# Kernel optimization log

Hardware: AMD Instinct MI355X
Metric: run time of the kernel (lower is better)

Reference implementation:

```python
import jax, jax.numpy as jnp
import numpy as np

B, S, D, H = 2, 2048, 2048, 16
HD = D // H
ROPE_BASE = 10000.0
N_DOCS = 8


def setup_inputs() -> dict:
    key = jax.random.key(0)
    ks = jax.random.split(key, 7)
    scale = 1.0 / np.sqrt(D)
    x = jax.random.normal(ks[0], (B, S, D), dtype=jnp.float32)
    doc_ids = jnp.sort(jax.random.randint(ks[1], (B, S), 0, N_DOCS), axis=1)
    Wq = jax.random.normal(ks[2], (D, D), dtype=jnp.float32) * scale
    Wk = jax.random.normal(ks[3], (D, D), dtype=jnp.float32) * scale
    Wv = jax.random.normal(ks[4], (D, D), dtype=jnp.float32) * scale
    Wo = jax.random.normal(ks[5], (D, D), dtype=jnp.float32) * scale
    bo = jax.random.normal(ks[6], (D,), dtype=jnp.float32) * 0.01
    return {"x": x, "doc_ids": doc_ids, "Wq": Wq, "Wk": Wk, "Wv": Wv, "Wo": Wo, "bo": bo}


def _rotate_half(t):
    # interleaved pairs: (x0,x1,x2,x3,...) -> (-x1,x0,-x3,x2,...)
    t1 = t[..., 0::2]
    t2 = t[..., 1::2]
    return jnp.stack((-t2, t1), axis=-1).reshape(t.shape)


def _doc_position_ids(doc_ids):
    b, s = doc_ids.shape
    boundary = jnp.concatenate(
        [jnp.ones((b, 1), dtype=bool), doc_ids[:, 1:] != doc_ids[:, :-1]], axis=1)
    ar = jnp.arange(s)[None, :]
    boundary_pos = jnp.where(boundary, ar, 0)
    last_boundary = jax.lax.cummax(boundary_pos, axis=1)
    return ar - last_boundary  # position within each document


def reference(x, doc_ids, Wq, Wk, Wv, Wo, bo):
    b, s, d = x.shape
    h, hd = H, HD

    q = (x @ Wq).reshape(b, s, h, hd).transpose(0, 2, 1, 3)  # [b,h,s,hd]
    k = (x @ Wk).reshape(b, s, h, hd).transpose(0, 2, 1, 3)
    v = (x @ Wv).reshape(b, s, h, hd).transpose(0, 2, 1, 3)

    # doc-aware RoPE: positions reset at document boundaries
    pos = _doc_position_ids(doc_ids).astype(jnp.float32)  # [b,s]
    inv_freq = 1.0 / (ROPE_BASE ** (jnp.arange(0, hd, 2, dtype=jnp.float32) / hd))
    freqs = pos[..., None] * inv_freq  # [b,s,hd/2]
    cos = jnp.repeat(jnp.cos(freqs), 2, axis=-1)[:, None]  # [b,1,s,hd]
    sin = jnp.repeat(jnp.sin(freqs), 2, axis=-1)[:, None]
    q = q * cos + _rotate_half(q) * sin
    k = k * cos + _rotate_half(k) * sin

    scores = jnp.einsum("bhqd,bhkd->bhqk", q, k)
    # doc-blockwise causal mask: attend only to j<=i within same document
    same_doc = doc_ids[:, :, None] == doc_ids[:, None, :]  # [b,s,s] (i,j)
    allowed = jnp.tril(same_doc)[:, None]  # [b,1,s,s]
    inv_scale = 1.0 / np.sqrt(hd)
    scores = jnp.where(allowed, scores * inv_scale, -jnp.inf)
    attn = jax.nn.softmax(scores, axis=-1)

    ctx = jnp.einsum("bhqk,bhkd->bhqd", attn, v)
    ctx = ctx.transpose(0, 2, 1, 3).reshape(b, s, d)
    return ctx @ Wo + bo
```

## Files before the change

kernel.cpp:

```cpp
#include <hip/hip_runtime.h>
#include <hip/hip_bf16.h>

#define Dd 2048
#define Ss 2048
#define Bb 2
#define Hh 16
#define HDd 128
#define BSs (Bb*Ss)
#define NTILES 32

typedef __bf16 bf16;
typedef __bf16 bf16x8 __attribute__((ext_vector_type(8)));
typedef __bf16 bf16x4 __attribute__((ext_vector_type(4)));
typedef float f32x4 __attribute__((ext_vector_type(4)));

__device__ __forceinline__ void gload_lds16(const void* g, void* l) {
  __builtin_amdgcn_global_load_lds((__attribute__((address_space(1))) void*)(g),
                                   (__attribute__((address_space(3))) void*)(l), 16, 0, 0);
}

template <int N>
__device__ __forceinline__ void waitv() {
  if constexpr (N == 0) asm volatile("s_waitcnt vmcnt(0)" ::: "memory");
  else if constexpr (N == 2) asm volatile("s_waitcnt vmcnt(2)" ::: "memory");
  else if constexpr (N == 4) asm volatile("s_waitcnt vmcnt(4)" ::: "memory");
  else if constexpr (N == 6) asm volatile("s_waitcnt vmcnt(6)" ::: "memory");
  else if constexpr (N == 8) asm volatile("s_waitcnt vmcnt(8)" ::: "memory");
  else if constexpr (N == 10) asm volatile("s_waitcnt vmcnt(10)" ::: "memory");
}

__global__ void k_cvtx(const float* __restrict__ x, bf16* __restrict__ xb) {
  int i = (blockIdx.x * 256 + threadIdx.x) * 4;
  f32x4 v = *(const f32x4*)(x + i);
  bf16x4 o;
  o[0] = (bf16)v[0]; o[1] = (bf16)v[1]; o[2] = (bf16)v[2]; o[3] = (bf16)v[3];
  *(bf16x4*)(xb + i) = o;
}

__global__ void k_tw(const float* __restrict__ W0, const float* __restrict__ W1,
                     const float* __restrict__ W2, const float* __restrict__ W3,
                     bf16* __restrict__ T0, bf16* __restrict__ T1,
                     bf16* __restrict__ T2, bf16* __restrict__ T3) {
  const float* W; bf16* T;
  switch (blockIdx.z) {
    case 0: W = W0; T = T0; break;
    case 1: W = W1; T = T1; break;
    case 2: W = W2; T = T2; break;
    default: W = W3; T = T3; break;
  }
  __shared__ float t[64][65];
  int n0 = blockIdx.x * 64, k0 = blockIdx.y * 64;
  int tid = threadIdx.x;
#pragma unroll
  for (int rr = 0; rr < 4; rr++) {
    int r = (tid >> 4) + rr * 16;
    f32x4 vv = *(const f32x4*)(W + (size_t)(k0 + r) * Dd + n0 + (tid & 15) * 4);
#pragma unroll
    for (int j = 0; j < 4; j++) t[r][(tid & 15) * 4 + j] = vv[j];
  }
  __syncthreads();
#pragma unroll
  for (int rr = 0; rr < 4; rr++) {
    int n = rr * 16 + (tid >> 4);
    int kb = (tid & 15) * 4;
    bf16x4 o;
#pragma unroll
    for (int j = 0; j < 4; j++) o[j] = (bf16)t[kb + j][n];
    *(bf16x4*)(T + (size_t)(n0 + n) * Dd + k0 + kb) = o;
  }
}

__global__ void k_pos(const int* __restrict__ doc, int* __restrict__ pos) {
  int b = blockIdx.x;
  __shared__ int bp[2][Ss];
  const int* db = doc + (size_t)b * Ss;
  for (int i = threadIdx.x; i < Ss; i += 1024) {
    int bd = (i == 0) || (db[i] != db[i - 1]);
    bp[0][i] = bd ? i : 0;
  }
  __syncthreads();
  int src = 0;
  for (int off = 1; off < Ss; off <<= 1) {
    for (int i = threadIdx.x; i < Ss; i += 1024) {
      int v = bp[src][i];
      if (i >= off) v = max(v, bp[src][i - off]);
      bp[1 - src][i] = v;
    }
    __syncthreads();
    src = 1 - src;
  }
  for (int i = threadIdx.x; i < Ss; i += 1024)
    pos[(size_t)b * Ss + i] = i - bp[src][i];
}

__device__ __forceinline__ bf16x8 lds_frag(const char* buf, int row, int cb) {
  return *(const bf16x8*)(buf + row * 128 + (cb ^ ((row & 7) << 4)));
}

__device__ __forceinline__ void stage_slot128(const bf16* gA, const bf16* gB,
                                              int m0, int n0, int t, int slot, int buf,
                                              char* AL, char* BL, int tid) {
  const char* gp; char* l; int rbase;
  char* bufA = AL + (size_t)buf * 16384;
  char* bufB = BL + (size_t)buf * 32768;
  if (slot == 0)      { gp = (const char*)gA; l = bufA;         rbase = m0; }
  else if (slot == 1) { gp = (const char*)gB; l = bufB;         rbase = n0; }
  else                { gp = (const char*)gB; l = bufB + 16384; rbase = n0 + 128; }
  int ktb = t * 128;
#pragma unroll
  for (int p = 0; p < 2; p++) {
    int o = p * 8192 + tid * 16;
    int r = o >> 7, cb = o & 127;
    gload_lds16(gp + (size_t)(rbase + r) * 4096 + ktb + (cb ^ ((r & 7) << 4)), l + o);
  }
}

template <bool STAGE, int WV0, int WV1>
__device__ __forceinline__ void do_tile128(const bf16* gA, const bf16* gB, int m0, int n0,
                                           int t, int bi, int b2, char* AL, char* BL, int tid,
                                           int wr, int wc, int ln, int g,
                                           f32x4 acc[4][4]) {
  const char* tileA = AL + (size_t)bi * 16384;
  const char* tileB = BL + (size_t)bi * 32768;
  bf16x8 af[4][2], bf_[2][2];

#pragma unroll
  for (int mq = 0; mq < 4; mq++)
#pragma unroll
    for (int kk = 0; kk < 2; kk++)
      af[mq][kk] = lds_frag(tileA, wr * 64 + mq * 16 + ln, kk * 64 + g * 16);
#pragma unroll
  for (int nq = 0; nq < 2; nq++)
#pragma unroll
    for (int kk = 0; kk < 2; kk++)
      bf_[nq][kk] = lds_frag(tileB, wc * 32 + nq * 16 + ln, kk * 64 + g * 16);
  if (STAGE) {
    stage_slot128(gA, gB, m0, n0, t + 2, 0, b2, AL, BL, tid);
    stage_slot128(gA, gB, m0, n0, t + 2, 1, b2, AL, BL, tid);
  }
  waitv<WV0>();
  __builtin_amdgcn_s_barrier();
  __builtin_amdgcn_s_setprio(1);
#pragma unroll
  for (int mq = 0; mq < 4; mq++)
#pragma unroll
    for (int nq = 0; nq < 2; nq++)
#pragma unroll
      for (int kk = 0; kk < 2; kk++)
        acc[mq][nq] = __builtin_amdgcn_mfma_f32_16x16x32_bf16(af[mq][kk], bf_[nq][kk], acc[mq][nq], 0, 0, 0);
  __builtin_amdgcn_s_setprio(0);
  __builtin_amdgcn_s_barrier();

#pragma unroll
  for (int nq = 0; nq < 2; nq++)
#pragma unroll
    for (int kk = 0; kk < 2; kk++)
      bf_[nq][kk] = lds_frag(tileB, 128 + wc * 32 + nq * 16 + ln, kk * 64 + g * 16);
  if (STAGE)
    stage_slot128(gA, gB, m0, n0, t + 2, 2, b2, AL, BL, tid);
  waitv<WV1>();
  __builtin_amdgcn_s_barrier();
  __builtin_amdgcn_s_setprio(1);
#pragma unroll
  for (int mq = 0; mq < 4; mq++)
#pragma unroll
    for (int nq = 0; nq < 2; nq++)
#pragma unroll
      for (int kk = 0; kk < 2; kk++)
        acc[mq][2 + nq] = __builtin_amdgcn_mfma_f32_16x16x32_bf16(af[mq][kk], bf_[nq][kk], acc[mq][2 + nq], 0, 0, 0);
  __builtin_amdgcn_s_setprio(0);
  __builtin_amdgcn_s_barrier();
}

__device__ __forceinline__ void gemm128_core(const bf16* gA, const bf16* gB,
                                             int m0, int n0, char* AL, char* BL,
                                             f32x4 acc[4][4]) {
  const int tid = threadIdx.x;
  const int l = tid & 63, w = tid >> 6;
  const int wr = w >> 2, wc = w & 3;
  const int g = l >> 4, ln = l & 15;
  f32x4 z = {0.f, 0.f, 0.f, 0.f};
#pragma unroll
  for (int i = 0; i < 4; i++)
#pragma unroll
    for (int n = 0; n < 4; n++) acc[i][n] = z;

  stage_slot128(gA, gB, m0, n0, 0, 0, 0, AL, BL, tid);
  stage_slot128(gA, gB, m0, n0, 0, 1, 0, AL, BL, tid);
  stage_slot128(gA, gB, m0, n0, 0, 2, 0, AL, BL, tid);
  stage_slot128(gA, gB, m0, n0, 1, 0, 1, AL, BL, tid);
  stage_slot128(gA, gB, m0, n0, 1, 1, 1, AL, BL, tid);
  stage_slot128(gA, gB, m0, n0, 1, 2, 1, AL, BL, tid);
  waitv<8>();
  __builtin_amdgcn_s_barrier();

  int bi = 0, b2 = 2;
  for (int t = 0; t < NTILES - 2; t++) {
    do_tile128<true, 10, 8>(gA, gB, m0, n0, t, bi, b2, AL, BL, tid, wr, wc, ln, g, acc);
    bi = (bi == 2) ? 0 : bi + 1;
    b2 = (b2 == 2) ? 0 : b2 + 1;
  }
  do_tile128<false, 6, 2>(gA, gB, m0, n0, NTILES - 2, bi, 0, AL, BL, tid, wr, wc, ln, g, acc);
  bi = (bi == 2) ? 0 : bi + 1;
  do_tile128<false, 0, -1>(gA, gB, m0, n0, NTILES - 1, bi, 0, AL, BL, tid, wr, wc, ln, g, acc);
}

__global__ __launch_bounds__(512, 2) void k_qkv128(const bf16* __restrict__ xb,
                                                   const bf16* __restrict__ wqkvt,
                                                   const int* __restrict__ pos,
                                                   bf16* __restrict__ q,
                                                   bf16* __restrict__ k,
                                                   bf16* __restrict__ vt) {
  __shared__ char SLM[147456];
  char* AL = SLM;
  char* BL = SLM + 49152;
  int bid = blockIdx.x;
  int idx = (bid & 7) * 96 + (bid >> 3);
  int mt = idx / 24, nt = idx % 24;
  int m0 = mt * 128, n0 = nt * 256;

  f32x4 acc[4][4];
  gemm128_core(xb, wqkvt, m0, n0, AL, BL, acc);

  const int tid = threadIdx.x;
  const int l = tid & 63, w = tid >> 6;
  const int wr = w >> 2, wc = w & 3, g = l >> 4, ln = l & 15;
  int z = n0 >> 11;
  int n0l = n0 & 2047;
  int bix = m0 >> 11;
  int sl0 = m0 & 2047;

  if (z == 2) {
#pragma unroll
    for (int mq = 0; mq < 4; mq++) {
      int sl = sl0 + wr * 64 + mq * 16 + g * 4;
#pragma unroll
      for (int ni = 0; ni < 4; ni++) {
        int col = n0l + (ni >> 1) * 128 + wc * 32 + (ni & 1) * 16 + ln;
        int h = col >> 7, hd = col & 127;
        bf16x4 o;
#pragma unroll
        for (int r2 = 0; r2 < 4; r2++) o[r2] = (bf16)acc[mq][ni][r2];
        *(bf16x4*)(vt + (((size_t)(bix * Hh + h) * HDd + hd) * Ss + sl)) = o;
      }
    }
  } else {
    bf16* dst = (z == 0) ? q : k;
    float* T = (float*)SLM;
    const float c1 = 0.14391156642398168f;
    int cg = (tid & 31) * 8;
    int hb = n0l + cg;
    int hh = hb >> 7, hd0 = hb & 127;
    float fr[4];
#pragma unroll
    for (int pr = 0; pr < 4; pr++)
      fr[pr] = __expf(-(float)((hd0 >> 1) + pr) * c1);

#pragma unroll
    for (int pass = 0; pass < 2; pass++) {
      __syncthreads();
      if (wr == pass) {
#pragma unroll
        for (int mq = 0; mq < 4; mq++) {
#pragma unroll
          for (int ni = 0; ni < 4; ni++) {
            int c = (ni >> 1) * 128 + wc * 32 + (ni & 1) * 16 + ln;
            int rb = mq * 16 + g * 4;
#pragma unroll
            for (int r2 = 0; r2 < 4; r2++)
              T[(rb + r2) * 260 + c] = acc[mq][ni][r2];
          }
        }
      }
      __syncthreads();
#pragma unroll
      for (int j = 0; j < 4; j++) {
        int r = j * 16 + (tid >> 5);
        int sg = m0 + pass * 64 + r;
        float p = (float)pos[sg];
        f32x4 v0 = *(const f32x4*)(T + r * 260 + cg);
        f32x4 v1 = *(const f32x4*)(T + r * 260 + cg + 4);
        float e0[4] = {v0[0], v0[2], v1[0], v1[2]};
        float e1[4] = {v0[1], v0[3], v1[1], v1[3]};
        int s = sg & 2047;
        bf16x8 o;
#pragma unroll
        for (int pr = 0; pr < 4; pr++) {
          float ang = p * fr[pr];
          float sn, cs;
          __sincosf(ang, &sn, &cs);
          o[2 * pr]     = (bf16)(e0[pr] * cs - e1[pr] * sn);
          o[2 * pr + 1] = (bf16)(e1[pr] * cs + e0[pr] * sn);
        }
        *(bf16x8*)(dst + (((size_t)(bix * Hh + hh) * Ss + s) * HDd + hd0)) = o;
      }
    }
  }
}

__global__ __launch_bounds__(512, 2) void k_out128(const bf16* __restrict__ ctx,
                                                   const bf16* __restrict__ wot,
                                                   const float* __restrict__ bo,
                                                   float* __restrict__ outp) {
  __shared__ char AL[49152];
  __shared__ char BL[98304];
  int bid = blockIdx.x;
  int x = bid & 7, j = bid >> 3;
  int mt = (x >> 1) * 8 + (j >> 2);
  int nt = (x & 1) * 4 + (j & 3);
  int m0 = mt * 128, n0 = nt * 256;

  f32x4 acc[4][4];
  gemm128_core(ctx, wot, m0, n0, AL, BL, acc);

  const int l = threadIdx.x & 63, w = threadIdx.x >> 6;
  const int wr = w >> 2, wc = w & 3, g = l >> 4, ln = l & 15;
  float bov[4];
#pragma unroll
  for (int ni = 0; ni < 4; ni++)
    bov[ni] = bo[n0 + (ni >> 1) * 128 + wc * 32 + (ni & 1) * 16 + ln];
#pragma unroll
  for (int mq = 0; mq < 4; mq++)
#pragma unroll
    for (int r2 = 0; r2 < 4; r2++) {
      int row = m0 + wr * 64 + mq * 16 + g * 4 + r2;
#pragma unroll
      for (int ni = 0; ni < 4; ni++) {
        int col = n0 + (ni >> 1) * 128 + wc * 32 + (ni & 1) * 16 + ln;
        outp[(size_t)row * Dd + col] = acc[mq][ni][r2] + bov[ni];
      }
    }
}

__global__ __launch_bounds__(256) void k_attn(const bf16* __restrict__ q,
                                              const bf16* __restrict__ k,
                                              const bf16* __restrict__ vt,
                                              const int* __restrict__ pos,
                                              bf16* __restrict__ ctx) {
  __shared__ bf16 Ks[64 * 128];
  __shared__ bf16 Vts[128 * 64];
  __shared__ bf16 Pw[4][16 * 64];
  int bh = blockIdx.y;
  int b = bh >> 4, h = bh & 15;
  int qt = blockIdx.x, q0 = qt * 64;
  const int tid = threadIdx.x, l = tid & 63, w = tid >> 6, g = l >> 4, ln = l & 15;
  const bf16* qb = q + (size_t)bh * Ss * HDd;
  const bf16* kb = k + (size_t)bh * Ss * HDd;
  const bf16* vb = vt + (size_t)bh * Ss * HDd;

  bf16x8 qf[4];
  int qr = q0 + w * 16 + ln;
#pragma unroll
  for (int ks = 0; ks < 4; ks++)
    qf[ks] = *(const bf16x8*)(qb + (size_t)qr * HDd + ks * 32 + 8 * g);

  int rrow[4], dstart[4];
  float m[4], lsum[4];
#pragma unroll
  for (int r2 = 0; r2 < 4; r2++) {
    rrow[r2] = q0 + w * 16 + 4 * g + r2;
    dstart[r2] = rrow[r2] - pos[(size_t)b * Ss + rrow[r2]];
    m[r2] = -1e30f;
    lsum[r2] = 0.f;
  }
  f32x4 oacc[8];
  f32x4 z = {0.f, 0.f, 0.f, 0.f};
#pragma unroll
  for (int n = 0; n < 8; n++) oacc[n] = z;

  int kt_start = (q0 - pos[(size_t)b * Ss + q0]) >> 6;
  const float iscale = 0.08838834764831845f;

  for (int kt = kt_start; kt <= qt; kt++) {
    int kv0 = kt * 64;
#pragma unroll
    for (int i2 = 0; i2 < 4; i2++) {
      int o = i2 * 4096 + w * 1024 + l * 16;
      int rk = o >> 8, cbk = o & 255;
      gload_lds16((const char*)kb + (size_t)(kv0 + rk) * 256 + cbk,
                  (char*)Ks + i2 * 4096 + w * 1024);
      int rv = o >> 7, cbv = o & 127;
      gload_lds16((const char*)vb + (size_t)rv * (Ss * 2) + (size_t)kv0 * 2 + cbv,
                  (char*)Vts + i2 * 4096 + w * 1024);
    }
    __syncthreads();

    f32x4 sc[4];
#pragma unroll
    for (int n = 0; n < 4; n++) {
      f32x4 a = z;
#pragma unroll
      for (int ks = 0; ks < 4; ks++) {
        bf16x8 bfrag = *(const bf16x8*)(Ks + (n * 16 + ln) * 128 + ks * 32 + 8 * g);
        a = __builtin_amdgcn_mfma_f32_16x16x32_bf16(qf[ks], bfrag, a, 0, 0, 0);
      }
      sc[n] = a;
    }

    float pmax[4] = {-1e30f, -1e30f, -1e30f, -1e30f};
    float pv[4][4];
#pragma unroll
    for (int n = 0; n < 4; n++) {
      int kvc = kv0 + n * 16 + ln;
#pragma unroll
      for (int r2 = 0; r2 < 4; r2++) {
        bool ok = (kvc <= rrow[r2]) && (kvc >= dstart[r2]);
        float sv = ok ? sc[n][r2] * iscale : -1e30f;
        pv[n][r2] = sv;
        pmax[r2] = fmaxf(pmax[r2], sv);
      }
    }
#pragma unroll
    for (int off = 1; off < 16; off <<= 1)
#pragma unroll
      for (int r2 = 0; r2 < 4; r2++)
        pmax[r2] = fmaxf(pmax[r2], __shfl_xor(pmax[r2], off, 64));

    float alpha[4];
#pragma unroll
    for (int r2 = 0; r2 < 4; r2++) {
      float mn = fmaxf(m[r2], pmax[r2]);
      alpha[r2] = __expf(m[r2] - mn);
      m[r2] = mn;
    }

    float rs[4] = {0.f, 0.f, 0.f, 0.f};
#pragma unroll
    for (int n = 0; n < 4; n++) {
      int kvc = kv0 + n * 16 + ln;
#pragma unroll
      for (int r2 = 0; r2 < 4; r2++) {
        bool ok = (kvc <= rrow[r2]) && (kvc >= dstart[r2]);
        float p = ok ? __expf(pv[n][r2] - m[r2]) : 0.f;
        rs[r2] += p;
        Pw[w][(4 * g + r2) * 64 + n * 16 + ln] = (bf16)p;
      }
    }
#pragma unroll
    for (int off = 1; off < 16; off <<= 1)
#pragma unroll
      for (int r2 = 0; r2 < 4; r2++) rs[r2] += __shfl_xor(rs[r2], off, 64);
#pragma unroll
    for (int r2 = 0; r2 < 4; r2++) lsum[r2] = lsum[r2] * alpha[r2] + rs[r2];
#pragma unroll
    for (int n = 0; n < 8; n++)
#pragma unroll
      for (int r2 = 0; r2 < 4; r2++) oacc[n][r2] *= alpha[r2];
    __syncthreads();

#pragma unroll
    for (int n = 0; n < 8; n++) {
#pragma unroll
      for (int ks = 0; ks < 2; ks++) {
        bf16x8 pa = *(const bf16x8*)(&Pw[w][ln * 64 + ks * 32 + 8 * g]);
        bf16x8 vfr = *(const bf16x8*)(Vts + (n * 16 + ln) * 64 + ks * 32 + 8 * g);
        oacc[n] = __builtin_amdgcn_mfma_f32_16x16x32_bf16(pa, vfr, oacc[n], 0, 0, 0);
      }
    }
    __syncthreads();
  }

#pragma unroll
  for (int n = 0; n < 8; n++)
#pragma unroll
    for (int r2 = 0; r2 < 4; r2++) {
      float val = oacc[n][r2] / lsum[r2];
      ctx[((size_t)(b * Ss + rrow[r2])) * Dd + h * HDd + n * 16 + ln] = (bf16)val;
    }
}

extern "C" void kernel_launch(void* const* d_in, const int* in_sizes, int n_in,
                              void* d_out, int out_size, void* d_ws, size_t ws_size,
                              hipStream_t stream) {
  const float* x = (const float*)d_in[0];
  const int* doc = (const int*)d_in[1];
  const float* Wq = (const float*)d_in[2];
  const float* Wk = (const float*)d_in[3];
  const float* Wv = (const float*)d_in[4];
  const float* Wo = (const float*)d_in[5];
  const float* bo = (const float*)d_in[6];
  float* outp = (float*)d_out;

  char* ws = (char*)d_ws;
  size_t off = 0;
  auto alloc = [&](size_t bytes) {
    char* p = ws + off;
    off += (bytes + 255) & ~(size_t)255;
    return p;
  };
  bf16* xb = (bf16*)alloc((size_t)BSs * Dd * 2);
  bf16* wqkvt = (bf16*)alloc((size_t)3 * Dd * Dd * 2);
  bf16* wot = (bf16*)alloc((size_t)Dd * Dd * 2);
  bf16* qd = (bf16*)alloc((size_t)BSs * Dd * 2);
  bf16* kd = (bf16*)alloc((size_t)BSs * Dd * 2);
  bf16* vtd = (bf16*)alloc((size_t)BSs * Dd * 2);
  bf16* ctxd = (bf16*)alloc((size_t)BSs * Dd * 2);
  int* pos = (int*)alloc((size_t)BSs * 4);

  k_cvtx<<<(BSs * Dd) / 1024, 256, 0, stream>>>(x, xb);
  k_tw<<<dim3(Dd / 64, Dd / 64, 4), 256, 0, stream>>>(
      Wq, Wk, Wv, Wo, wqkvt, wqkvt + (size_t)Dd * Dd, wqkvt + (size_t)2 * Dd * Dd, wot);
  k_pos<<<Bb, 1024, 0, stream>>>(doc, pos);
  k_qkv128<<<dim3(768), 512, 0, stream>>>(xb, wqkvt, pos, qd, kd, vtd);
  k_attn<<<dim3(Ss / 64, Bb * Hh), 256, 0, stream>>>(qd, kd, vtd, pos, ctxd);
  k_out128<<<dim3(256), 512, 0, stream>>>(ctxd, wot, bo, outp);
}
```

Before: 227.0 us.

## Restructure GEMM main loop into single-phase tiles with one barrier per k-step

Replaces the two-phase per-k-tile GEMM schedule (separate B halves, two barriers and two waits) with one stage of the full A and B tiles per k-step. Each warp now reads four A and four B fragments per k-half and issues a 4x4 MFMA block, with a single vmcnt wait and barrier per tile. The loop is unrolled by three to fix triple-buffer indices, and the output-GEMM block-to-tile mapping changes. This aims to cut barrier and wait overhead, at the cost of higher register pressure and less overlap of loads with compute inside a tile.

```diff
diff --git a/kernel.cpp b/kernel.cpp
--- a/kernel.cpp
+++ b/kernel.cpp
@@ -7,7 +7,7 @@
 #define Hh 16
 #define HDd 128
 #define BSs (Bb*Ss)
-#define NTILES 32
+#define NTIL 32
 
 typedef __bf16 bf16;
 typedef __bf16 bf16x8 __attribute__((ext_vector_type(8)));
@@ -22,11 +22,7 @@
 template <int N>
 __device__ __forceinline__ void waitv() {
   if constexpr (N == 0) asm volatile("s_waitcnt vmcnt(0)" ::: "memory");
-  else if constexpr (N == 2) asm volatile("s_waitcnt vmcnt(2)" ::: "memory");
-  else if constexpr (N == 4) asm volatile("s_waitcnt vmcnt(4)" ::: "memory");
   else if constexpr (N == 6) asm volatile("s_waitcnt vmcnt(6)" ::: "memory");
-  else if constexpr (N == 8) asm volatile("s_waitcnt vmcnt(8)" ::: "memory");
-  else if constexpr (N == 10) asm volatile("s_waitcnt vmcnt(10)" ::: "memory");
 }
 
 __global__ void k_cvtx(const float* __restrict__ x, bf16* __restrict__ xb) {
@@ -93,88 +89,64 @@
     pos[(size_t)b * Ss + i] = i - bp[src][i];
 }
 
-__device__ __forceinline__ bf16x8 lds_frag(const char* buf, int row, int cb) {
-  return *(const bf16x8*)(buf + row * 128 + (cb ^ ((row & 7) << 4)));
-}
-
-__device__ __forceinline__ void stage_slot128(const bf16* gA, const bf16* gB,
-                                              int m0, int n0, int t, int slot, int buf,
-                                              char* AL, char* BL, int tid) {
-  const char* gp; char* l; int rbase;
-  char* bufA = AL + (size_t)buf * 16384;
-  char* bufB = BL + (size_t)buf * 32768;
-  if (slot == 0)      { gp = (const char*)gA; l = bufA;         rbase = m0; }
-  else if (slot == 1) { gp = (const char*)gB; l = bufB;         rbase = n0; }
-  else                { gp = (const char*)gB; l = bufB + 16384; rbase = n0 + 128; }
+__device__ __forceinline__ void stage64(const char* gA, const char* gB,
+                                        int m0, int n0, int t, int buf,
+                                        char* AL, char* BL, int tid) {
   int ktb = t * 128;
 #pragma unroll
   for (int p = 0; p < 2; p++) {
     int o = p * 8192 + tid * 16;
     int r = o >> 7, cb = o & 127;
-    gload_lds16(gp + (size_t)(rbase + r) * 4096 + ktb + (cb ^ ((r & 7) << 4)), l + o);
-  }
-}
-
-template <bool STAGE, int WV0, int WV1>
-__device__ __forceinline__ void do_tile128(const bf16* gA, const bf16* gB, int m0, int n0,
-                                           int t, int bi, int b2, char* AL, char* BL, int tid,
-                                           int wr, int wc, int ln, int g,
-                                           f32x4 acc[4][4]) {
-  const char* tileA = AL + (size_t)bi * 16384;
-  const char* tileB = BL + (size_t)bi * 32768;
-  bf16x8 af[4][2], bf_[2][2];
-
-#pragma unroll
-  for (int mq = 0; mq < 4; mq++)
-#pragma unroll
-    for (int kk = 0; kk < 2; kk++)
-      af[mq][kk] = lds_frag(tileA, wr * 64 + mq * 16 + ln, kk * 64 + g * 16);
-#pragma unroll
-  for (int nq = 0; nq < 2; nq++)
-#pragma unroll
-    for (int kk = 0; kk < 2; kk++)
-      bf_[nq][kk] = lds_frag(tileB, wc * 32 + nq * 16 + ln, kk * 64 + g * 16);
-  if (STAGE) {
-    stage_slot128(gA, gB, m0, n0, t + 2, 0, b2, AL, BL, tid);
-    stage_slot128(gA, gB, m0, n0, t + 2, 1, b2, AL, BL, tid);
-  }
-  waitv<WV0>();
+    gload_lds16(gA + (size_t)(m0 + r) * 4096 + ktb + (cb ^ ((r & 7) << 4)),
+                AL + buf * 16384 + o);
+  }
+#pragma unroll
+  for (int p = 0; p < 4; p++) {
+    int o = p * 8192 + tid * 16;
+    int r = o >> 7, cb = o & 127;
+    gload_lds16(gB + (size_t)(n0 + r) * 4096 + ktb + (cb ^ ((r & 7) << 4)),
+                BL + buf * 32768 + o);
+  }
+}
+
+template <bool STAGE, int WV>
+__device__ __forceinline__ void do_tile64(const char* gA, const char* gB, int m0, int n0,
+                                          int t, int bi, int b2, char* AL, char* BL, int tid,
+                                          int wr, int wc, int ln, int g,
+                                          f32x4 (&acc)[4][4]) {
+  if (STAGE) stage64(gA, gB, m0, n0, t + 2, b2, AL, BL, tid);
+  const char* tA = AL + bi * 16384;
+  const char* tB = BL + bi * 32768;
+#pragma unroll
+  for (int kk = 0; kk < 2; kk++) {
+    bf16x8 af[4], bf[4];
+#pragma unroll
+    for (int mq = 0; mq < 4; mq++) {
+      int row = wr * 64 + mq * 16 + ln;
+      af[mq] = *(const bf16x8*)(tA + row * 128 + ((kk * 64 + g * 16) ^ ((row & 7) << 4)));
+    }
+#pragma unroll
+    for (int nq = 0; nq < 4; nq++) {
+      int row = wc * 64 + nq * 16 + ln;
+      bf[nq] = *(const bf16x8*)(tB + row * 128 + ((kk * 64 + g * 16) ^ ((row & 7) << 4)));
+    }
+    __builtin_amdgcn_s_setprio(1);
+#pragma unroll
+    for (int mq = 0; mq < 4; mq++)
+#pragma unroll
+      for (int nq = 0; nq < 4; nq++)
+        acc[mq][nq] = __builtin_amdgcn_mfma_f32_16x16x32_bf16(af[mq], bf[nq], acc[mq][nq], 0, 0, 0);
+    __builtin_amdgcn_s_setprio(0);
+  }
+  waitv<WV>();
   __builtin_amdgcn_s_barrier();
-  __builtin_amdgcn_s_setprio(1);
-#pragma unroll
-  for (int mq = 0; mq < 4; mq++)
-#pragma unroll
-    for (int nq = 0; nq < 2; nq++)
-#pragma unroll
-      for (int kk = 0; kk < 2; kk++)
-        acc[mq][nq] = __builtin_amdgcn_mfma_f32_16x16x32_bf16(af[mq][kk], bf_[nq][kk], acc[mq][nq], 0, 0, 0);
-  __builtin_amdgcn_s_setprio(0);
-  __builtin_amdgcn_s_barrier();
-
-#pragma unroll
-  for (int nq = 0; nq < 2; nq++)
-#pragma unroll
-    for (int kk = 0; kk < 2; kk++)
-      bf_[nq][kk] = lds_frag(tileB, 128 + wc * 32 + nq * 16 + ln, kk * 64 + g * 16);
-  if (STAGE)
-    stage_slot128(gA, gB, m0, n0, t + 2, 2, b2, AL, BL, tid);
-  waitv<WV1>();
-  __builtin_amdgcn_s_barrier();
-  __builtin_amdgcn_s_setprio(1);
-#pragma unroll
-  for (int mq = 0; mq < 4; mq++)
-#pragma unroll
-    for (int nq = 0; nq < 2; nq++)
-#pragma unroll
-      for (int kk = 0; kk < 2; kk++)
-        acc[mq][2 + nq] = __builtin_amdgcn_mfma_f32_16x16x32_bf16(af[mq][kk], bf_[nq][kk], acc[mq][2 + nq], 0, 0, 0);
-  __builtin_amdgcn_s_setprio(0);
-  __builtin_amdgcn_s_barrier();
-}
-
-__device__ __forceinline__ void gemm128_core(const bf16* gA, const bf16* gB,
-                                             int m0, int n0, char* AL, char* BL,
-                                             f32x4 acc[4][4]) {
+}
+
+__device__ __forceinline__ void gemm64_core(const bf16* gA_, const bf16* gB_,
+                                            int m0, int n0, char* AL, char* BL,
+                                            f32x4 (&acc)[4][4]) {
+  const char* gA = (const char*)gA_;
+  const char* gB = (const char*)gB_;
   const int tid = threadIdx.x;
   const int l = tid & 63, w = tid >> 6;
   const int wr = w >> 2, wc = w & 3;
@@ -185,27 +157,22 @@
 #pragma unroll
     for (int n = 0; n < 4; n++) acc[i][n] = z;
 
-  stage_slot128(gA, gB, m0, n0, 0, 0, 0, AL, BL, tid);
-  stage_slot128(gA, gB, m0, n0, 0, 1, 0, AL, BL, tid);
-  stage_slot128(gA, gB, m0, n0, 0, 2, 0, AL, BL, tid);
-  stage_slot128(gA, gB, m0, n0, 1, 0, 1, AL, BL, tid);
-  stage_slot128(gA, gB, m0, n0, 1, 1, 1, AL, BL, tid);
-  stage_slot128(gA, gB, m0, n0, 1, 2, 1, AL, BL, tid);
-  waitv<8>();
+  stage64(gA, gB, m0, n0, 0, 0, AL, BL, tid);
+  stage64(gA, gB, m0, n0, 1, 1, AL, BL, tid);
+  waitv<6>();
   __builtin_amdgcn_s_barrier();
 
-  int bi = 0, b2 = 2;
-  for (int t = 0; t < NTILES - 2; t++) {
-    do_tile128<true, 10, 8>(gA, gB, m0, n0, t, bi, b2, AL, BL, tid, wr, wc, ln, g, acc);
-    bi = (bi == 2) ? 0 : bi + 1;
-    b2 = (b2 == 2) ? 0 : b2 + 1;
-  }
-  do_tile128<false, 6, 2>(gA, gB, m0, n0, NTILES - 2, bi, 0, AL, BL, tid, wr, wc, ln, g, acc);
-  bi = (bi == 2) ? 0 : bi + 1;
-  do_tile128<false, 0, -1>(gA, gB, m0, n0, NTILES - 1, bi, 0, AL, BL, tid, wr, wc, ln, g, acc);
-}
-
-__global__ __launch_bounds__(512, 2) void k_qkv128(const bf16* __restrict__ xb,
+  for (int tt = 0; tt < 10; tt++) {
+    int t = tt * 3;
+    do_tile64<true, 6>(gA, gB, m0, n0, t,     0, 2, AL, BL, tid, wr, wc, ln, g, acc);
+    do_tile64<true, 6>(gA, gB, m0, n0, t + 1, 1, 0, AL, BL, tid, wr, wc, ln, g, acc);
+    do_tile64<true, 6>(gA, gB, m0, n0, t + 2, 2, 1, AL, BL, tid, wr, wc, ln, g, acc);
+  }
+  do_tile64<false, 0>(gA, gB, m0, n0, 30, 0, 0, AL, BL, tid, wr, wc, ln, g, acc);
+  do_tile64<false, -1>(gA, gB, m0, n0, 31, 1, 0, AL, BL, tid, wr, wc, ln, g, acc);
+}
+
+__global__ __launch_bounds__(512, 2) void k_qkv256(const bf16* __restrict__ xb,
                                                    const bf16* __restrict__ wqkvt,
                                                    const int* __restrict__ pos,
                                                    bf16* __restrict__ q,
@@ -220,7 +187,7 @@
   int m0 = mt * 128, n0 = nt * 256;
 
   f32x4 acc[4][4];
-  gemm128_core(xb, wqkvt, m0, n0, AL, BL, acc);
+  gemm64_core(xb, wqkvt, m0, n0, AL, BL, acc);
 
   const int tid = threadIdx.x;
   const int l = tid & 63, w = tid >> 6;
@@ -235,12 +202,12 @@
     for (int mq = 0; mq < 4; mq++) {
       int sl = sl0 + wr * 64 + mq * 16 + g * 4;
 #pragma unroll
-      for (int ni = 0; ni < 4; ni++) {
-        int col = n0l + (ni >> 1) * 128 + wc * 32 + (ni & 1) * 16 + ln;
+      for (int nq = 0; nq < 4; nq++) {
+        int col = n0l + wc * 64 + nq * 16 + ln;
         int h = col >> 7, hd = col & 127;
         bf16x4 o;
 #pragma unroll
-        for (int r2 = 0; r2 < 4; r2++) o[r2] = (bf16)acc[mq][ni][r2];
+        for (int r2 = 0; r2 < 4; r2++) o[r2] = (bf16)acc[mq][nq][r2];
         *(bf16x4*)(vt + (((size_t)(bix * Hh + h) * HDd + hd) * Ss + sl)) = o;
       }
     }
@@ -263,12 +230,12 @@
 #pragma unroll
         for (int mq = 0; mq < 4; mq++) {
 #pragma unroll
-          for (int ni = 0; ni < 4; ni++) {
-            int c = (ni >> 1) * 128 + wc * 32 + (ni & 1) * 16 + ln;
+          for (int nq = 0; nq < 4; nq++) {
+            int c = wc * 64 + nq * 16 + ln;
             int rb = mq * 16 + g * 4;
 #pragma unroll
             for (int r2 = 0; r2 < 4; r2++)
-              T[(rb + r2) * 260 + c] = acc[mq][ni][r2];
+              T[(rb + r2) * 260 + c] = acc[mq][nq][r2];
           }
         }
       }
@@ -298,36 +265,35 @@
   }
 }
 
-__global__ __launch_bounds__(512, 2) void k_out128(const bf16* __restrict__ ctx,
+__global__ __launch_bounds__(512, 2) void k_out256(const bf16* __restrict__ ctx,
                                                    const bf16* __restrict__ wot,
                                                    const float* __restrict__ bo,
                                                    float* __restrict__ outp) {
   __shared__ char AL[49152];
   __shared__ char BL[98304];
   int bid = blockIdx.x;
-  int x = bid & 7, j = bid >> 3;
-  int mt = (x >> 1) * 8 + (j >> 2);
-  int nt = (x & 1) * 4 + (j & 3);
+  int idx = (bid & 7) * 32 + (bid >> 3);
+  int mt = idx >> 3, nt = idx & 7;
   int m0 = mt * 128, n0 = nt * 256;
 
   f32x4 acc[4][4];
-  gemm128_core(ctx, wot, m0, n0, AL, BL, acc);
+  gemm64_core(ctx, wot, m0, n0, AL, BL, acc);
 
   const int l = threadIdx.x & 63, w = threadIdx.x >> 6;
   const int wr = w >> 2, wc = w & 3, g = l >> 4, ln = l & 15;
   float bov[4];
 #pragma unroll
-  for (int ni = 0; ni < 4; ni++)
-    bov[ni] = bo[n0 + (ni >> 1) * 128 + wc * 32 + (ni & 1) * 16 + ln];
+  for (int nq = 0; nq < 4; nq++)
+    bov[nq] = bo[n0 + wc * 64 + nq * 16 + ln];
 #pragma unroll
   for (int mq = 0; mq < 4; mq++)
 #pragma unroll
     for (int r2 = 0; r2 < 4; r2++) {
       int row = m0 + wr * 64 + mq * 16 + g * 4 + r2;
 #pragma unroll
-      for (int ni = 0; ni < 4; ni++) {
-        int col = n0 + (ni >> 1) * 128 + wc * 32 + (ni & 1) * 16 + ln;
-        outp[(size_t)row * Dd + col] = acc[mq][ni][r2] + bov[ni];
+      for (int nq = 0; nq < 4; nq++) {
+        int col = n0 + wc * 64 + nq * 16 + ln;
+        outp[(size_t)row * Dd + col] = acc[mq][nq][r2] + bov[nq];
       }
     }
 }
@@ -501,7 +467,7 @@
   k_tw<<<dim3(Dd / 64, Dd / 64, 4), 256, 0, stream>>>(
       Wq, Wk, Wv, Wo, wqkvt, wqkvt + (size_t)Dd * Dd, wqkvt + (size_t)2 * Dd * Dd, wot);
   k_pos<<<Bb, 1024, 0, stream>>>(doc, pos);
-  k_qkv128<<<dim3(768), 512, 0, stream>>>(xb, wqkvt, pos, qd, kd, vtd);
+  k_qkv256<<<dim3(768), 512, 0, stream>>>(xb, wqkvt, pos, qd, kd, vtd);
   k_attn<<<dim3(Ss / 64, Bb * Hh), 256, 0, stream>>>(qd, kd, vtd, pos, ctxd);
-  k_out128<<<dim3(256), 512, 0, stream>>>(ctxd, wot, bo, outp);
-}
+  k_out256<<<dim3(256), 512, 0, stream>>>(ctxd, wot, bo, outp);
+}
```

New measurement: 224.2 us. Within noise of the previous version (-1.3%).
